# Optimization experiments

Hardware: AMD Instinct MI355X
Metric: run time of the kernel (lower is better)

Reference implementation:

```python
import jax, jax.numpy as jnp
import numpy as np

TEMP = 0.07
BASE_TEMP = 0.07
LOSS_WEIGHT = 0.5
BN_EPS = 1e-5


def _embed(x, w1, b1, gamma, beta, w2, b2):
    # 1x1 conv C->C  (x: [N,C,H,W], w1: [C_out,C_in])
    h = jnp.einsum('nchw,oc->nohw', x, w1) + b1[None, :, None, None]
    # BatchNorm2d in training mode: batch stats over (N,H,W), biased variance
    mean = h.mean(axis=(0, 2, 3), keepdims=True)
    var = h.var(axis=(0, 2, 3), keepdims=True)
    h = (h - mean) * jax.lax.rsqrt(var + BN_EPS)
    h = h * gamma[None, :, None, None] + beta[None, :, None, None]
    h = jax.nn.relu(h)
    h = jnp.einsum('nchw,oc->nohw', h, w2) + b2[None, :, None, None]
    # F.normalize(p=2, dim=1) with eps=1e-12
    nrm = jnp.sqrt(jnp.sum(h * h, axis=1, keepdims=True))
    return h / jnp.maximum(nrm, 1e-12)


def _contrastive(feats_, labels_):
    # feats_: [T, n_view, C]; labels_: [T]
    T, n_view, C = feats_.shape
    mask_small = (labels_[:, None] == labels_[None, :]).astype(feats_.dtype)  # [T,T]
    # torch.cat(torch.unbind(feats_, dim=1), dim=0): view-major ordering
    cf = feats_.transpose(1, 0, 2).reshape(T * n_view, C)
    logits = (cf @ cf.T) / TEMP                                   # [M,M], M=T*n_view
    logits = logits - jax.lax.stop_gradient(jnp.max(logits, axis=1, keepdims=True))
    mask = jnp.tile(mask_small, (n_view, n_view))                  # repeat(anchor_count, contrast_count)
    neg_mask = 1.0 - mask                                          # computed BEFORE diagonal removal
    M = T * n_view
    logits_mask = 1.0 - jnp.eye(M, dtype=feats_.dtype)
    mask = mask * logits_mask
    exp_logits = jnp.exp(logits)
    neg_logits = jnp.sum(exp_logits * neg_mask, axis=1, keepdims=True)
    log_prob = logits - jnp.log(exp_logits + neg_logits)
    mean_log_prob_pos = jnp.sum(mask * log_prob, axis=1) / (jnp.sum(mask, axis=1) + 1e-6)
    loss = -(TEMP / BASE_TEMP) * mean_log_prob_pos
    return jnp.mean(loss)


def setup_inputs() -> dict:
    N, C_in, H, W = 8, 512, 128, 128
    feat_dim, num_classes = 256, 19
    max_views, max_samples, ignore_label = 100, 1024, -1
    rng = np.random.RandomState(0)

    preds_S = rng.randn(N, C_in, H, W).astype(np.float32)
    # gt label map already at (H,W) => nearest interpolation is identity
    gt = rng.randint(0, num_classes, (N, H * W))
    logits_S = rng.randn(N, num_classes, H * W).astype(np.float32)
    predict = logits_S.argmax(axis=1)  # [N, H*W]

    # ---- replicate _hard_anchor_sampling on host (fixed seed) ----
    classes, total = [], 0
    for i in range(N):
        cl = [int(c) for c in np.unique(gt[i])
              if c != ignore_label and (gt[i] == c).sum() > max_views]
        classes.append(cl)
        total += len(cl)
    n_view = min(max_samples // total, max_views)

    b_idx, p_idx, y_cls = [], [], []
    for i in range(N):
        for c in classes[i]:
            hard = np.where((predict[i] == c) & (gt[i] != c))[0]
            easy = np.where((predict[i] == c) & (gt[i] == c))[0]
            nh, ne = len(hard), len(easy)
            if nh >= n_view / 2 and ne >= n_view / 2:
                kh = n_view // 2; ke = n_view - kh
            elif nh >= n_view / 2:
                ke = ne; kh = n_view - ke
            else:
                kh = nh; ke = n_view - kh
            hs = hard[rng.permutation(nh)[:kh]]
            es = easy[rng.permutation(ne)[:ke]]
            b_idx.append(i)
            p_idx.append(np.concatenate([hs, es]))
            y_cls.append(c)

    batch_idx = jnp.asarray(np.array(b_idx), dtype=jnp.int32)          # [T]
    pix_idx = jnp.asarray(np.stack(p_idx), dtype=jnp.int32)            # [T, n_view]
    y_cls = jnp.asarray(np.array(y_cls), dtype=jnp.int32)              # [T]

    def p(shape, scale, k):
        r = np.random.RandomState(k)
        return jnp.asarray((r.randn(*shape) * scale).astype(np.float32))

    return {
        'preds_S': jnp.asarray(preds_S),
        'w1': p((C_in, C_in), 0.02, 1),
        'b1': jnp.zeros((C_in,), jnp.float32),
        'gamma': jnp.ones((C_in,), jnp.float32),
        'beta': jnp.zeros((C_in,), jnp.float32),
        'w2': p((feat_dim, C_in), 0.02, 2),
        'b2': jnp.zeros((feat_dim,), jnp.float32),
        'batch_idx': batch_idx,
        'pix_idx': pix_idx,
        'y_cls': y_cls,
    }


def reference(preds_S, w1, b1, gamma, beta, w2, b2, batch_idx, pix_idx, y_cls):
    f = _embed(preds_S, w1, b1, gamma, beta, w2, b2)        # [N, C, H, W]
    N, C, H, W = f.shape
    feats = f.transpose(0, 2, 3, 1).reshape(N, H * W, C)     # [N, HW, C]
    X_ = feats[batch_idx[:, None], pix_idx]                   # [T, n_view, C]
    labels_ = y_cls.astype(f.dtype)
    return LOSS_WEIGHT * _contrastive(X_, labels_)
```

## Files before the change

### kernel.cpp

```cpp
#include <hip/hip_runtime.h>
#include <hip/hip_bf16.h>

#define C_IN   512
#define C_OUT  256
#define HW     16384
#define NIMG   8
#define PTOT   (NIMG * HW)
#define MP     1024
#define TEMP_INV (1.0f / 0.07f)
#define BN_EPS   1e-5f
#define SPB    4
#define OGRP   4
#define IGRP   4
#define BK     64
#define KCH    2048
#define NCHUNK (PTOT / KCH)

typedef float  f32x4  __attribute__((ext_vector_type(4)));
typedef short  short8 __attribute__((ext_vector_type(8)));
typedef short  short4v __attribute__((ext_vector_type(4)));

#define WS_S1   0
#define WS_G    (WS_S1 + NIMG * C_IN)
#define WS_W1P  (WS_G + C_IN * C_IN)
#define WS_B1P  (WS_W1P + C_IN * C_IN)
#define WS_CF   (WS_B1P + C_IN)
#define WS_XB_F (WS_CF + MP * C_OUT)
#define WS_NEED_FAST ((size_t)WS_XB_F * 4 + (size_t)PTOT * C_IN * 2)
#define WS_PART_F (WS_XB_F + PTOT * (C_IN / 2))
#define NPART_F   (10 * NCHUNK * 128 * 128)
#define WS_NEED_PART ((size_t)(WS_PART_F + NPART_F) * 4)

__global__ __launch_bounds__(256)
void kprep(const float* __restrict__ x, __hip_bfloat16* __restrict__ xb,
           float* __restrict__ s1p, float* __restrict__ out) {
    int plane = blockIdx.x;
    if (plane == 0 && threadIdx.x == 0) *out = 0.f;
    const float4* p = (const float4*)(x + (size_t)plane * HW);
    short4v* q = (short4v*)(xb + (size_t)plane * HW);
    float acc = 0.f;
    for (int i = threadIdx.x; i < HW / 4; i += 256) {
        float4 v = p[i];
        acc += v.x + v.y + v.z + v.w;
        union { short4v s; __hip_bfloat162 h[2]; } u;
        u.h[0] = __float22bfloat162_rn(make_float2(v.x, v.y));
        u.h[1] = __float22bfloat162_rn(make_float2(v.z, v.w));
        q[i] = u.s;
    }
    for (int off = 32; off; off >>= 1) acc += __shfl_down(acc, off, 64);
    __shared__ float red[4];
    int lane = threadIdx.x & 63, wv = threadIdx.x >> 6;
    if (lane == 0) red[wv] = acc;
    __syncthreads();
    if (threadIdx.x == 0)
        s1p[plane] = red[0] + red[1] + red[2] + red[3];
}

__global__ __launch_bounds__(256)
void ksum(const float* __restrict__ x, float* __restrict__ s1p, float* __restrict__ out) {
    int plane = blockIdx.x;
    if (plane == 0 && threadIdx.x == 0) *out = 0.f;
    const float4* p = (const float4*)(x + (size_t)plane * HW);
    float acc = 0.f;
    for (int i = threadIdx.x; i < HW / 4; i += 256) {
        float4 v = p[i];
        acc += v.x + v.y + v.z + v.w;
    }
    for (int off = 32; off; off >>= 1) acc += __shfl_down(acc, off, 64);
    __shared__ float red[4];
    int lane = threadIdx.x & 63, wv = threadIdx.x >> 6;
    if (lane == 0) red[wv] = acc;
    __syncthreads();
    if (threadIdx.x == 0)
        s1p[plane] = red[0] + red[1] + red[2] + red[3];
}

__device__ const int TI2[10] = {0,1,2,3, 0,0,0,1,1,2};
__device__ const int TJ2[10] = {0,1,2,3, 1,2,3,2,3,3};

template<bool PART>
__global__ __launch_bounds__(256, 3)
void kgram2(const __hip_bfloat16* __restrict__ xb, float* __restrict__ G,
            float* __restrict__ Gp) {
    __shared__ __hip_bfloat16 buf[2][128 * BK];
    int tile  = blockIdx.x;
    int IT = TI2[tile] * 128;
    int JT = TJ2[tile] * 128;
    bool diag = (IT == JT);
    int bsel = diag ? 0 : 1;
    int chunk = blockIdx.y;
    int n   = chunk >> 3;
    int hw0 = (chunk & 7) * KCH;
    int wave = threadIdx.x >> 6;
    int lane = threadIdx.x & 63;
    int wi = wave >> 1, wj = wave & 1;

    const __hip_bfloat16* gA = xb + ((size_t)n * C_IN + IT) * HW + hw0;
    const __hip_bfloat16* gB = xb + ((size_t)n * C_IN + JT) * HW + hw0;

    int rrel = lane >> 3;
    int slot = lane & 7;

    f32x4 acc[4][4];
#pragma unroll
    for (int i = 0; i < 4; ++i)
#pragma unroll
        for (int j = 0; j < 4; ++j) acc[i][j] = {0.f, 0.f, 0.f, 0.f};

    int m  = lane & 15;
    int kq = lane >> 4;

#pragma unroll 1
    for (int s = 0; s < KCH / BK; ++s) {
        int kk = s * BK;
#pragma unroll
        for (int i_ = 0; i_ < 4; ++i_) {
            int row = wave * 32 + i_ * 8 + rrel;
            int g   = slot ^ (row & 7);
            __builtin_amdgcn_global_load_lds(
                (const __attribute__((address_space(1))) void*)
                    (gA + (size_t)row * HW + kk + g * 8),
                (__attribute__((address_space(3))) void*)
                    (&buf[0][(wave * 32 + i_ * 8) * BK]),
                16, 0, 0);
            if (!diag)
                __builtin_amdgcn_global_load_lds(
                    (const __attribute__((address_space(1))) void*)
                        (gB + (size_t)row * HW + kk + g * 8),
                    (__attribute__((address_space(3))) void*)
                        (&buf[1][(wave * 32 + i_ * 8) * BK]),
                    16, 0, 0);
        }
        __syncthreads();
#pragma unroll
        for (int h = 0; h < 2; ++h) {
            short8 af[4], bf[4];
#pragma unroll
            for (int t_ = 0; t_ < 4; ++t_) {
                int ra = wi * 64 + t_ * 16 + m;
                int qa = (h * 4 + kq) ^ (ra & 7);
                af[t_] = *(const short8*)&buf[0][ra * BK + qa * 8];
                int rb = wj * 64 + t_ * 16 + m;
                int qb = (h * 4 + kq) ^ (rb & 7);
                bf[t_] = *(const short8*)&buf[bsel][rb * BK + qb * 8];
            }
#pragma unroll
            for (int i_ = 0; i_ < 4; ++i_)
#pragma unroll
                for (int j_ = 0; j_ < 4; ++j_)
                    acc[i_][j_] = __builtin_amdgcn_mfma_f32_16x16x32_bf16(
                        af[i_], bf[j_], acc[i_][j_], 0, 0, 0);
        }
        __syncthreads();
    }

    int r0 = (lane >> 4) * 4;
    int cc = lane & 15;
    if (PART) {
        float* P = Gp + ((size_t)tile * NCHUNK + chunk) * (128 * 128);
#pragma unroll
        for (int i = 0; i < 4; ++i)
#pragma unroll
            for (int j = 0; j < 4; ++j)
#pragma unroll
                for (int r = 0; r < 4; ++r)
                    P[(wi * 64 + i * 16 + r0 + r) * 128 + (wj * 64 + j * 16 + cc)]
                        = acc[i][j][r];
    } else {
#pragma unroll
        for (int i = 0; i < 4; ++i)
#pragma unroll
            for (int j = 0; j < 4; ++j)
#pragma unroll
                for (int r = 0; r < 4; ++r)
                    atomicAdd(&G[(size_t)(IT + wi * 64 + i * 16 + r0 + r) * C_IN
                                 + (JT + wj * 64 + j * 16 + cc)],
                              acc[i][j][r]);
    }
}

__global__ __launch_bounds__(256)
void kgacc(const float* __restrict__ Gp, float* __restrict__ G) {
    int tile = blockIdx.x >> 4;
    int seg  = blockIdx.x & 15;
    int IT = TI2[tile] * 128, JT = TJ2[tile] * 128;
    int e0 = seg * 1024 + threadIdx.x * 4;
    const float* base = Gp + (size_t)tile * NCHUNK * (128 * 128) + e0;
    f32x4 a0 = {0,0,0,0}, a1 = {0,0,0,0}, a2 = {0,0,0,0}, a3 = {0,0,0,0};
    for (int ch = 0; ch < NCHUNK; ch += 4) {
        a0 += *(const f32x4*)(base + (size_t)(ch + 0) * (128 * 128));
        a1 += *(const f32x4*)(base + (size_t)(ch + 1) * (128 * 128));
        a2 += *(const f32x4*)(base + (size_t)(ch + 2) * (128 * 128));
        a3 += *(const f32x4*)(base + (size_t)(ch + 3) * (128 * 128));
    }
    f32x4 s = (a0 + a1) + (a2 + a3);
    int r = e0 >> 7, c = e0 & 127;
    *(f32x4*)(&G[(size_t)(IT + r) * C_IN + JT + c]) = s;
    if (IT != JT) {
#pragma unroll
        for (int k = 0; k < 4; ++k)
            G[(size_t)(JT + c + k) * C_IN + IT + r] = s[k];
    }
}

__global__ __launch_bounds__(256)
void kmirror(float* __restrict__ G) {
    int i = blockIdx.x;
    for (int j = threadIdx.x; j < C_IN; j += 256) {
        if ((i >> 7) > (j >> 7))
            G[(size_t)i * C_IN + j] = G[(size_t)j * C_IN + i];
    }
}

__device__ inline short8 load_frag_f32(const float* p) {
    float4 a = *(const float4*)p;
    float4 b = *(const float4*)(p + 4);
    union { short8 s; __hip_bfloat162 h[4]; } u;
    u.h[0] = __float22bfloat162_rn(make_float2(a.x, a.y));
    u.h[1] = __float22bfloat162_rn(make_float2(a.z, a.w));
    u.h[2] = __float22bfloat162_rn(make_float2(b.x, b.y));
    u.h[3] = __float22bfloat162_rn(make_float2(b.z, b.w));
    return u.s;
}

__global__ __launch_bounds__(256)
void kgram_f32(const float* __restrict__ x, float* __restrict__ G) {
    int bz  = blockIdx.z;
    int n   = bz >> 2;
    int hw0 = (bz & 3) * 4096;
    int wave = threadIdx.x >> 6;
    int lane = threadIdx.x & 63;
    int wi = wave >> 1, wj = wave & 1;
    int I0 = blockIdx.x * 128 + wi * 64;
    int J0 = blockIdx.y * 128 + wj * 64;
    int m    = lane & 15;
    int koff = (lane >> 4) * 8;

    const float* baseA[4];
    const float* baseB[4];
#pragma unroll
    for (int t = 0; t < 4; ++t) {
        baseA[t] = x + ((size_t)n * C_IN + (I0 + t * 16 + m)) * HW + hw0 + koff;
        baseB[t] = x + ((size_t)n * C_IN + (J0 + t * 16 + m)) * HW + hw0 + koff;
    }

    f32x4 acc[4][4];
#pragma unroll
    for (int i = 0; i < 4; ++i)
#pragma unroll
        for (int j = 0; j < 4; ++j) acc[i][j] = {0.f, 0.f, 0.f, 0.f};

    for (int kk = 0; kk < 4096; kk += 32) {
        short8 afr[4], bfr[4];
#pragma unroll
        for (int t = 0; t < 4; ++t) {
            afr[t] = load_frag_f32(baseA[t] + kk);
            bfr[t] = load_frag_f32(baseB[t] + kk);
        }
#pragma unroll
        for (int i = 0; i < 4; ++i)
#pragma unroll
            for (int j = 0; j < 4; ++j)
                acc[i][j] = __builtin_amdgcn_mfma_f32_16x16x32_bf16(
                    afr[i], bfr[j], acc[i][j], 0, 0, 0);
    }

    int r0 = (lane >> 4) * 4;
    int cc = lane & 15;
#pragma unroll
    for (int i = 0; i < 4; ++i)
#pragma unroll
        for (int j = 0; j < 4; ++j)
#pragma unroll
            for (int r = 0; r < 4; ++r)
                atomicAdd(&G[(size_t)(I0 + i * 16 + r0 + r) * C_IN + (J0 + j * 16 + cc)],
                          acc[i][j][r]);
}

__global__ __launch_bounds__(256)
void kstats(const float* __restrict__ w1, const float* __restrict__ b1,
            const float* __restrict__ gamma, const float* __restrict__ beta,
            const float* __restrict__ s1p, const float* __restrict__ G,
            float* __restrict__ w1p, float* __restrict__ b1p) {
    int o0 = blockIdx.x * OGRP;
    int tid = threadIdx.x;
    __shared__ float wr[OGRP][C_IN];
    __shared__ float redd[4][OGRP];
    __shared__ float redq[4][OGRP];
    __shared__ float alpha_s[OGRP];

    for (int idx = tid; idx < OGRP * C_IN; idx += 256) {
        int og = idx >> 9, c = idx & (C_IN - 1);
        wr[og][c] = w1[(size_t)(o0 + og) * C_IN + c];
    }
    __syncthreads();

    float dot1[OGRP], quad[OGRP];
#pragma unroll
    for (int og = 0; og < OGRP; ++og) { dot1[og] = 0.f; quad[og] = 0.f; }

    for (int c = tid; c < C_IN; c += 256) {
        const float* gr = G + (size_t)c * C_IN;
        float s1c = 0.f;
#pragma unroll
        for (int nn = 0; nn < NIMG; ++nn) s1c += s1p[nn * C_IN + c];
        float inner[OGRP];
#pragma unroll
        for (int og = 0; og < OGRP; ++og) inner[og] = 0.f;
        for (int d = 0; d < C_IN; d += 4) {
            float4 gv = *(const float4*)(gr + d);
#pragma unroll
            for (int og = 0; og < OGRP; ++og) {
                float4 wv = *(const float4*)(&wr[og][d]);
                inner[og] += gv.x * wv.x + gv.y * wv.y + gv.z * wv.z + gv.w * wv.w;
            }
        }
#pragma unroll
        for (int og = 0; og < OGRP; ++og) {
            float wc = wr[og][c];
            quad[og] += inner[og] * wc;
            dot1[og] += s1c * wc;
        }
    }
#pragma unroll
    for (int og = 0; og < OGRP; ++og) {
        for (int off = 32; off; off >>= 1) {
            dot1[og] += __shfl_down(dot1[og], off, 64);
            quad[og] += __shfl_down(quad[og], off, 64);
        }
    }
    int lane = tid & 63, wv = tid >> 6;
    if (lane == 0) {
#pragma unroll
        for (int og = 0; og < OGRP; ++og) { redd[wv][og] = dot1[og]; redq[wv][og] = quad[og]; }
    }
    __syncthreads();
    if (tid < OGRP) {
        int og = tid;
        float d1 = redd[0][og] + redd[1][og] + redd[2][og] + redd[3][og];
        float q  = redq[0][og] + redq[1][og] + redq[2][og] + redq[3][og];
        float b  = b1[o0 + og];
        float mean = d1 / (float)PTOT + b;
        float eh2  = (q + 2.f * b * d1) / (float)PTOT + b * b;
        float var  = eh2 - mean * mean;
        float al   = gamma[o0 + og] * rsqrtf(var + BN_EPS);
        alpha_s[og] = al;
        b1p[o0 + og] = beta[o0 + og] + al * (b - mean);
    }
    __syncthreads();
    for (int idx = tid; idx < OGRP * C_IN; idx += 256) {
        int og = idx >> 9, c = idx & (C_IN - 1);
        w1p[(size_t)(o0 + og) * C_IN + c] = alpha_s[og] * wr[og][c];
    }
}

__global__ __launch_bounds__(256)
void kfeat(const float* __restrict__ x, const float* __restrict__ w1p,
           const float* __restrict__ b1p, const float* __restrict__ w2,
           const float* __restrict__ b2, const int* __restrict__ batch_idx,
           const int* __restrict__ pix_idx, float* __restrict__ cf,
           int M, int T, int n_view) {
    __shared__ float xcol[SPB][C_IN];
    __shared__ float h1[SPB][C_IN];
    __shared__ float fl[SPB][C_OUT];
    int tid = threadIdx.x;
    int m0 = blockIdx.x * SPB;

    for (int idx = tid; idx < SPB * C_IN; idx += 256) {
        int s = idx >> 9, c = idx & (C_IN - 1);
        int mm = m0 + s;
        float v = 0.f;
        if (mm < M) {
            int t = mm % T, vv = mm / T;
            int n = batch_idx[t];
            int pix = pix_idx[t * n_view + vv];
            v = x[((size_t)n * C_IN + c) * HW + pix];
        }
        xcol[s][c] = v;
    }
    __syncthreads();

    for (int o = tid; o < C_IN; o += 256) {
        float acc[SPB];
        float bb = b1p[o];
#pragma unroll
        for (int s = 0; s < SPB; ++s) acc[s] = bb;
        const float* wrp = w1p + (size_t)o * C_IN;
        for (int c = 0; c < C_IN; c += 4) {
            float4 w = *(const float4*)(wrp + c);
#pragma unroll
            for (int s = 0; s < SPB; ++s) {
                float4 xv = *(const float4*)(&xcol[s][c]);
                acc[s] += w.x * xv.x + w.y * xv.y + w.z * xv.z + w.w * xv.w;
            }
        }
#pragma unroll
        for (int s = 0; s < SPB; ++s) h1[s][o] = fmaxf(acc[s], 0.f);
    }
    __syncthreads();

    {
        int j = tid;
        float acc[SPB];
        float bb = b2[j];
#pragma unroll
        for (int s = 0; s < SPB; ++s) acc[s] = bb;
        const float* wrp = w2 + (size_t)j * C_IN;
        for (int o = 0; o < C_IN; o += 4) {
            float4 w = *(const float4*)(wrp + o);
#pragma unroll
            for (int s = 0; s < SPB; ++s) {
                float4 hv = *(const float4*)(&h1[s][o]);
                acc[s] += w.x * hv.x + w.y * hv.y + w.z * hv.z + w.w * hv.w;
            }
        }
#pragma unroll
        for (int s = 0; s < SPB; ++s) fl[s][j] = acc[s];
    }
    __syncthreads();

    int wv = tid >> 6, lane = tid & 63;
    {
        float sq = 0.f;
#pragma unroll
        for (int k = 0; k < 4; ++k) { float v = fl[wv][lane + 64 * k]; sq += v * v; }
        for (int off = 32; off; off >>= 1) sq += __shfl_down(sq, off, 64);
        float nrm = __shfl(sq, 0, 64);
        float rinv = 1.f / fmaxf(sqrtf(nrm), 1e-12f);
        int mm = m0 + wv;
        if (mm < M) {
#pragma unroll
            for (int k = 0; k < 4; ++k)
                cf[(size_t)mm * C_OUT + lane + 64 * k] = fl[wv][lane + 64 * k] * rinv;
        }
    }
}

__global__ __launch_bounds__(256)
void kloss(const float* __restrict__ cf, const int* __restrict__ y_cls,
           float* __restrict__ out, int M, int T) {
    int i0 = blockIdx.x * IGRP;
    int tid = threadIdx.x;
    __shared__ float ci[IGRP][C_OUT];
    __shared__ float row[IGRP][MP];
    __shared__ int   lbl[MP];
    __shared__ float redl[IGRP];
    int lane = tid & 63, wv = tid >> 6;

    for (int idx = tid; idx < IGRP * C_OUT; idx += 256) {
        int g = idx >> 8, c = idx & (C_OUT - 1);
        int ii = i0 + g;
        ci[g][c] = (ii < M) ? cf[(size_t)ii * C_OUT + c] : 0.f;
    }
    for (int j = tid; j < M; j += 256) lbl[j] = y_cls[j % T];
    __syncthreads();

    for (int j = tid; j < M; j += 256) {
        const float* cj = cf + (size_t)j * C_OUT;
        float acc[IGRP];
#pragma unroll
        for (int g = 0; g < IGRP; ++g) acc[g] = 0.f;
        for (int c = 0; c < C_OUT; c += 4) {
            float4 v = *(const float4*)(cj + c);
#pragma unroll
            for (int g = 0; g < IGRP; ++g) {
                float4 cv = *(const float4*)(&ci[g][c]);
                acc[g] += cv.x * v.x + cv.y * v.y + cv.z * v.z + cv.w * v.w;
            }
        }
#pragma unroll
        for (int g = 0; g < IGRP; ++g) row[g][j] = acc[g] * TEMP_INV;
    }
    __syncthreads();

    for (int g = wv; g < IGRP; g += 4) {
        int i = i0 + g;
        if (i < M) {
            int lbl_i = lbl[i];
            const float* r = row[g];

            float mx = -1e30f;
            for (int j = lane; j < M; j += 64) mx = fmaxf(mx, r[j]);
            for (int off = 32; off; off >>= 1) mx = fmaxf(mx, __shfl_down(mx, off, 64));
            mx = __shfl(mx, 0, 64);

            float neg = 0.f;
            for (int j = lane; j < M; j += 64)
                if (lbl[j] != lbl_i) neg += expf(r[j] - mx);
            for (int off = 32; off; off >>= 1) neg += __shfl_down(neg, off, 64);
            neg = __shfl(neg, 0, 64);

            float pos = 0.f; int cnt = 0;
            for (int j = lane; j < M; j += 64) {
                if (lbl[j] == lbl_i && j != i) {
                    float l = r[j] - mx;
                    pos += l - logf(expf(l) + neg);
                    cnt++;
                }
            }
            for (int off = 32; off; off >>= 1) {
                pos += __shfl_down(pos, off, 64);
                cnt += __shfl_down(cnt, off, 64);
            }
            if (lane == 0) redl[g] = -pos / ((float)cnt + 1e-6f);
        } else if (lane == 0) redl[g] = 0.f;
    }
    __syncthreads();
    if (tid == 0) {
        float s = 0.f;
        for (int g = 0; g < IGRP; ++g) s += redl[g];
        atomicAdd(out, s * (0.5f / (float)M));
    }
}

extern "C" void kernel_launch(void* const* d_in, const int* in_sizes, int n_in,
                              void* d_out, int out_size, void* d_ws, size_t ws_size,
                              hipStream_t stream) {
    const float* x     = (const float*)d_in[0];
    const float* w1    = (const float*)d_in[1];
    const float* b1    = (const float*)d_in[2];
    const float* gamma = (const float*)d_in[3];
    const float* beta  = (const float*)d_in[4];
    const float* w2    = (const float*)d_in[5];
    const float* b2    = (const float*)d_in[6];
    const int* batch_idx = (const int*)d_in[7];
    const int* pix_idx   = (const int*)d_in[8];
    const int* y_cls     = (const int*)d_in[9];

    int T = in_sizes[7];
    int M = in_sizes[8];
    int n_view = M / T;

    float* ws  = (float*)d_ws;
    float* s1p = ws + WS_S1;
    float* G   = ws + WS_G;
    float* w1p = ws + WS_W1P;
    float* b1p = ws + WS_B1P;
    float* cf  = ws + WS_CF;
    __hip_bfloat16* xb = (__hip_bfloat16*)(ws + WS_XB_F);
    float* Gpart = ws + WS_PART_F;

    if (ws_size >= WS_NEED_PART) {
        kprep<<<NIMG * C_IN, 256, 0, stream>>>(x, xb, s1p, (float*)d_out);
        kgram2<true><<<dim3(10, NCHUNK), 256, 0, stream>>>(xb, G, Gpart);
        kgacc<<<160, 256, 0, stream>>>(Gpart, G);
    } else if (ws_size >= WS_NEED_FAST) {
        hipMemsetAsync(G, 0, (size_t)(C_IN * C_IN) * sizeof(float), stream);
        kprep<<<NIMG * C_IN, 256, 0, stream>>>(x, xb, s1p, (float*)d_out);
        kgram2<false><<<dim3(10, NCHUNK), 256, 0, stream>>>(xb, G, nullptr);
        kmirror<<<C_IN, 256, 0, stream>>>(G);
    } else {
        hipMemsetAsync(G, 0, (size_t)(C_IN * C_IN) * sizeof(float), stream);
        ksum<<<NIMG * C_IN, 256, 0, stream>>>(x, s1p, (float*)d_out);
        kgram_f32<<<dim3(4, 4, 32), 256, 0, stream>>>(x, G);
    }
    kstats<<<C_IN / OGRP, 256, 0, stream>>>(w1, b1, gamma, beta, s1p, G, w1p, b1p);
    kfeat<<<(M + SPB - 1) / SPB, 256, 0, stream>>>(x, w1p, b1p, w2, b2,
                                                   batch_idx, pix_idx, cf, M, T, n_view);
    kloss<<<(M + IGRP - 1) / IGRP, 256, 0, stream>>>(cf, y_cls, (float*)d_out, M, T);
}
```

Before: 629.3 us.

## Double-buffer Gram kernel, XCD-aware block mapping, and parallelize BN stats

The partial-Gram kernel now double-buffers its LDS tiles, prefetching the next K-step while MFMAs run on the current one, and always loads separate A/B buffers. Blocks are remapped so the 8 chunks of a tile are spread across XCDs. The serial per-output kstats kernel is replaced by a 2D-parallel kquad reduction with atomics, a tiny kfin kernel, and folding of the BN scale into kfeat instead of writing a scaled W1 copy. Costs are more LDS per block (occupancy drops to 2), redundant B loads on diagonal tiles, and order-dependent float atomics.

```diff
diff --git a/kernel.cpp b/kernel.cpp
--- a/kernel.cpp
+++ b/kernel.cpp
@@ -10,32 +10,39 @@
 #define TEMP_INV (1.0f / 0.07f)
 #define BN_EPS   1e-5f
 #define SPB    4
-#define OGRP   4
 #define IGRP   4
 #define BK     64
 #define KCH    2048
 #define NCHUNK (PTOT / KCH)
+#define NTILE  10
 
 typedef float  f32x4  __attribute__((ext_vector_type(4)));
 typedef short  short8 __attribute__((ext_vector_type(8)));
 typedef short  short4v __attribute__((ext_vector_type(4)));
 
-#define WS_S1   0
-#define WS_G    (WS_S1 + NIMG * C_IN)
-#define WS_W1P  (WS_G + C_IN * C_IN)
-#define WS_B1P  (WS_W1P + C_IN * C_IN)
-#define WS_CF   (WS_B1P + C_IN)
-#define WS_XB_F (WS_CF + MP * C_OUT)
+#define WS_S1    0
+#define WS_G     (WS_S1 + NIMG * C_IN)
+#define WS_QUAD  (WS_G + C_IN * C_IN)
+#define WS_DOT1  (WS_QUAD + C_IN)
+#define WS_ALPHA (WS_DOT1 + C_IN)
+#define WS_B1P   (WS_ALPHA + C_IN)
+#define WS_CF    (WS_B1P + C_IN)
+#define WS_XB_F  (WS_CF + MP * C_OUT)
 #define WS_NEED_FAST ((size_t)WS_XB_F * 4 + (size_t)PTOT * C_IN * 2)
 #define WS_PART_F (WS_XB_F + PTOT * (C_IN / 2))
-#define NPART_F   (10 * NCHUNK * 128 * 128)
+#define NPART_F   (NTILE * NCHUNK * 128 * 128)
 #define WS_NEED_PART ((size_t)(WS_PART_F + NPART_F) * 4)
 
 __global__ __launch_bounds__(256)
 void kprep(const float* __restrict__ x, __hip_bfloat16* __restrict__ xb,
-           float* __restrict__ s1p, float* __restrict__ out) {
+           float* __restrict__ s1p, float* __restrict__ quadb,
+           float* __restrict__ dot1b, float* __restrict__ out) {
     int plane = blockIdx.x;
-    if (plane == 0 && threadIdx.x == 0) *out = 0.f;
+    if (plane == 0) {
+        if (threadIdx.x == 0) *out = 0.f;
+        quadb[threadIdx.x] = 0.f; quadb[256 + threadIdx.x] = 0.f;
+        dot1b[threadIdx.x] = 0.f; dot1b[256 + threadIdx.x] = 0.f;
+    }
     const float4* p = (const float4*)(x + (size_t)plane * HW);
     short4v* q = (short4v*)(xb + (size_t)plane * HW);
     float acc = 0.f;
@@ -57,9 +64,15 @@
 }
 
 __global__ __launch_bounds__(256)
-void ksum(const float* __restrict__ x, float* __restrict__ s1p, float* __restrict__ out) {
+void ksum(const float* __restrict__ x, float* __restrict__ s1p,
+          float* __restrict__ quadb, float* __restrict__ dot1b,
+          float* __restrict__ out) {
     int plane = blockIdx.x;
-    if (plane == 0 && threadIdx.x == 0) *out = 0.f;
+    if (plane == 0) {
+        if (threadIdx.x == 0) *out = 0.f;
+        quadb[threadIdx.x] = 0.f; quadb[256 + threadIdx.x] = 0.f;
+        dot1b[threadIdx.x] = 0.f; dot1b[256 + threadIdx.x] = 0.f;
+    }
     const float4* p = (const float4*)(x + (size_t)plane * HW);
     float acc = 0.f;
     for (int i = threadIdx.x; i < HW / 4; i += 256) {
@@ -75,31 +88,27 @@
         s1p[plane] = red[0] + red[1] + red[2] + red[3];
 }
 
-__device__ const int TI2[10] = {0,1,2,3, 0,0,0,1,1,2};
-__device__ const int TJ2[10] = {0,1,2,3, 1,2,3,2,3,3};
-
-template<bool PART>
-__global__ __launch_bounds__(256, 3)
-void kgram2(const __hip_bfloat16* __restrict__ xb, float* __restrict__ G,
-            float* __restrict__ Gp) {
-    __shared__ __hip_bfloat16 buf[2][128 * BK];
-    int tile  = blockIdx.x;
-    int IT = TI2[tile] * 128;
-    int JT = TJ2[tile] * 128;
-    bool diag = (IT == JT);
-    int bsel = diag ? 0 : 1;
-    int chunk = blockIdx.y;
+__device__ const int TI2[NTILE] = {0,1,2,3, 0,0,0,1,1,2};
+__device__ const int TJ2[NTILE] = {0,1,2,3, 1,2,3,2,3,3};
+
+__global__ __launch_bounds__(256, 2)
+void kgram3(const __hip_bfloat16* __restrict__ xb, float* __restrict__ Gp) {
+    __shared__ __hip_bfloat16 Ab[2][128 * BK];
+    __shared__ __hip_bfloat16 Bb[2][128 * BK];
+    int bid  = blockIdx.x;
+    int xcd  = bid & 7;
+    int r    = bid >> 3;
+    int tile = r % NTILE;
+    int chunk = (r / NTILE) * 8 + xcd;
+    int IT = TI2[tile] * 128, JT = TJ2[tile] * 128;
     int n   = chunk >> 3;
     int hw0 = (chunk & 7) * KCH;
-    int wave = threadIdx.x >> 6;
-    int lane = threadIdx.x & 63;
+    int wave = threadIdx.x >> 6, lane = threadIdx.x & 63;
     int wi = wave >> 1, wj = wave & 1;
-
     const __hip_bfloat16* gA = xb + ((size_t)n * C_IN + IT) * HW + hw0;
     const __hip_bfloat16* gB = xb + ((size_t)n * C_IN + JT) * HW + hw0;
-
-    int rrel = lane >> 3;
-    int slot = lane & 7;
+    int rrel = lane >> 3, slot = lane & 7;
+    int m = lane & 15, kq = lane >> 4;
 
     f32x4 acc[4][4];
 #pragma unroll
@@ -107,31 +116,24 @@
 #pragma unroll
         for (int j = 0; j < 4; ++j) acc[i][j] = {0.f, 0.f, 0.f, 0.f};
 
-    int m  = lane & 15;
-    int kq = lane >> 4;
-
-#pragma unroll 1
-    for (int s = 0; s < KCH / BK; ++s) {
-        int kk = s * BK;
+    auto stage = [&](int sel, int kk_) {
 #pragma unroll
         for (int i_ = 0; i_ < 4; ++i_) {
             int row = wave * 32 + i_ * 8 + rrel;
             int g   = slot ^ (row & 7);
             __builtin_amdgcn_global_load_lds(
                 (const __attribute__((address_space(1))) void*)
-                    (gA + (size_t)row * HW + kk + g * 8),
+                    (gA + (size_t)row * HW + kk_ + g * 8),
                 (__attribute__((address_space(3))) void*)
-                    (&buf[0][(wave * 32 + i_ * 8) * BK]),
-                16, 0, 0);
-            if (!diag)
-                __builtin_amdgcn_global_load_lds(
-                    (const __attribute__((address_space(1))) void*)
-                        (gB + (size_t)row * HW + kk + g * 8),
-                    (__attribute__((address_space(3))) void*)
-                        (&buf[1][(wave * 32 + i_ * 8) * BK]),
-                    16, 0, 0);
-        }
-        __syncthreads();
+                    (&Ab[sel][(wave * 32 + i_ * 8) * BK]), 16, 0, 0);
+            __builtin_amdgcn_global_load_lds(
+                (const __attribute__((address_space(1))) void*)
+                    (gB + (size_t)row * HW + kk_ + g * 8),
+                (__attribute__((address_space(3))) void*)
+                    (&Bb[sel][(wave * 32 + i_ * 8) * BK]), 16, 0, 0);
+        }
+    };
+    auto compute = [&](int cur) {
 #pragma unroll
         for (int h = 0; h < 2; ++h) {
             short8 af[4], bf[4];
@@ -139,10 +141,10 @@
             for (int t_ = 0; t_ < 4; ++t_) {
                 int ra = wi * 64 + t_ * 16 + m;
                 int qa = (h * 4 + kq) ^ (ra & 7);
-                af[t_] = *(const short8*)&buf[0][ra * BK + qa * 8];
+                af[t_] = *(const short8*)&Ab[cur][ra * BK + qa * 8];
                 int rb = wj * 64 + t_ * 16 + m;
                 int qb = (h * 4 + kq) ^ (rb & 7);
-                bf[t_] = *(const short8*)&buf[bsel][rb * BK + qb * 8];
+                bf[t_] = *(const short8*)&Bb[cur][rb * BK + qb * 8];
             }
 #pragma unroll
             for (int i_ = 0; i_ < 4; ++i_)
@@ -151,32 +153,36 @@
                     acc[i_][j_] = __builtin_amdgcn_mfma_f32_16x16x32_bf16(
                         af[i_], bf[j_], acc[i_][j_], 0, 0, 0);
         }
-        __syncthreads();
-    }
+    };
+
+    constexpr int NS = KCH / BK;
+    stage(0, 0);
+#pragma unroll 1
+    for (int s = 0; s < NS - 1; ++s) {
+        int cur = s & 1;
+        stage(cur ^ 1, (s + 1) * BK);
+        asm volatile("s_waitcnt vmcnt(8)" ::: "memory");
+        __builtin_amdgcn_sched_barrier(0);
+        __builtin_amdgcn_s_barrier();
+        compute(cur);
+        __builtin_amdgcn_s_barrier();
+    }
+    asm volatile("s_waitcnt vmcnt(0)" ::: "memory");
+    __builtin_amdgcn_sched_barrier(0);
+    __builtin_amdgcn_s_barrier();
+    compute((NS - 1) & 1);
 
     int r0 = (lane >> 4) * 4;
     int cc = lane & 15;
-    if (PART) {
-        float* P = Gp + ((size_t)tile * NCHUNK + chunk) * (128 * 128);
-#pragma unroll
-        for (int i = 0; i < 4; ++i)
-#pragma unroll
-            for (int j = 0; j < 4; ++j)
-#pragma unroll
-                for (int r = 0; r < 4; ++r)
-                    P[(wi * 64 + i * 16 + r0 + r) * 128 + (wj * 64 + j * 16 + cc)]
-                        = acc[i][j][r];
-    } else {
-#pragma unroll
-        for (int i = 0; i < 4; ++i)
-#pragma unroll
-            for (int j = 0; j < 4; ++j)
-#pragma unroll
-                for (int r = 0; r < 4; ++r)
-                    atomicAdd(&G[(size_t)(IT + wi * 64 + i * 16 + r0 + r) * C_IN
-                                 + (JT + wj * 64 + j * 16 + cc)],
-                              acc[i][j][r]);
-    }
+    float* P = Gp + ((size_t)tile * NCHUNK + chunk) * (128 * 128);
+#pragma unroll
+    for (int i = 0; i < 4; ++i)
+#pragma unroll
+        for (int j = 0; j < 4; ++j)
+#pragma unroll
+            for (int rr = 0; rr < 4; ++rr)
+                P[(wi * 64 + i * 16 + r0 + rr) * 128 + (wj * 64 + j * 16 + cc)]
+                    = acc[i][j][rr];
 }
 
 __global__ __launch_bounds__(256)
@@ -194,13 +200,91 @@
         a3 += *(const f32x4*)(base + (size_t)(ch + 3) * (128 * 128));
     }
     f32x4 s = (a0 + a1) + (a2 + a3);
-    int r = e0 >> 7, c = e0 & 127;
-    *(f32x4*)(&G[(size_t)(IT + r) * C_IN + JT + c]) = s;
+    int rr = e0 >> 7, c = e0 & 127;
+    *(f32x4*)(&G[(size_t)(IT + rr) * C_IN + JT + c]) = s;
     if (IT != JT) {
 #pragma unroll
         for (int k = 0; k < 4; ++k)
-            G[(size_t)(JT + c + k) * C_IN + IT + r] = s[k];
-    }
+            G[(size_t)(JT + c + k) * C_IN + IT + rr] = s[k];
+    }
+}
+
+__global__ __launch_bounds__(256, 3)
+void kgram_at(const __hip_bfloat16* __restrict__ xb, float* __restrict__ G) {
+    __shared__ __hip_bfloat16 buf[2][128 * BK];
+    int tile  = blockIdx.x;
+    int IT = TI2[tile] * 128, JT = TJ2[tile] * 128;
+    bool diag = (IT == JT);
+    int bsel = diag ? 0 : 1;
+    int chunk = blockIdx.y;
+    int n   = chunk >> 3;
+    int hw0 = (chunk & 7) * KCH;
+    int wave = threadIdx.x >> 6, lane = threadIdx.x & 63;
+    int wi = wave >> 1, wj = wave & 1;
+    const __hip_bfloat16* gA = xb + ((size_t)n * C_IN + IT) * HW + hw0;
+    const __hip_bfloat16* gB = xb + ((size_t)n * C_IN + JT) * HW + hw0;
+    int rrel = lane >> 3, slot = lane & 7;
+    int m = lane & 15, kq = lane >> 4;
+
+    f32x4 acc[4][4];
+#pragma unroll
+    for (int i = 0; i < 4; ++i)
+#pragma unroll
+        for (int j = 0; j < 4; ++j) acc[i][j] = {0.f, 0.f, 0.f, 0.f};
+
+#pragma unroll 1
+    for (int s = 0; s < KCH / BK; ++s) {
+        int kk = s * BK;
+#pragma unroll
+        for (int i_ = 0; i_ < 4; ++i_) {
+            int row = wave * 32 + i_ * 8 + rrel;
+            int g   = slot ^ (row & 7);
+            __builtin_amdgcn_global_load_lds(
+                (const __attribute__((address_space(1))) void*)
+                    (gA + (size_t)row * HW + kk + g * 8),
+                (__attribute__((address_space(3))) void*)
+                    (&buf[0][(wave * 32 + i_ * 8) * BK]), 16, 0, 0);
+            if (!diag)
+                __builtin_amdgcn_global_load_lds(
+                    (const __attribute__((address_space(1))) void*)
+                        (gB + (size_t)row * HW + kk + g * 8),
+                    (__attribute__((address_space(3))) void*)
+                        (&buf[1][(wave * 32 + i_ * 8) * BK]), 16, 0, 0);
+        }
+        __syncthreads();
+#pragma unroll
+        for (int h = 0; h < 2; ++h) {
+            short8 af[4], bf[4];
+#pragma unroll
+            for (int t_ = 0; t_ < 4; ++t_) {
+                int ra = wi * 64 + t_ * 16 + m;
+                int qa = (h * 4 + kq) ^ (ra & 7);
+                af[t_] = *(const short8*)&buf[0][ra * BK + qa * 8];
+                int rb = wj * 64 + t_ * 16 + m;
+                int qb = (h * 4 + kq) ^ (rb & 7);
+                bf[t_] = *(const short8*)&buf[bsel][rb * BK + qb * 8];
+            }
+#pragma unroll
+            for (int i_ = 0; i_ < 4; ++i_)
+#pragma unroll
+                for (int j_ = 0; j_ < 4; ++j_)
+                    acc[i_][j_] = __builtin_amdgcn_mfma_f32_16x16x32_bf16(
+                        af[i_], bf[j_], acc[i_][j_], 0, 0, 0);
+        }
+        __syncthreads();
+    }
+
+    int r0 = (lane >> 4) * 4;
+    int cc = lane & 15;
+#pragma unroll
+    for (int i = 0; i < 4; ++i)
+#pragma unroll
+        for (int j = 0; j < 4; ++j)
+#pragma unroll
+            for (int rr = 0; rr < 4; ++rr)
+                atomicAdd(&G[(size_t)(IT + wi * 64 + i * 16 + r0 + rr) * C_IN
+                             + (JT + wj * 64 + j * 16 + cc)],
+                          acc[i][j][rr]);
 }
 
 __global__ __launch_bounds__(256)
@@ -228,8 +312,7 @@
     int bz  = blockIdx.z;
     int n   = bz >> 2;
     int hw0 = (bz & 3) * 4096;
-    int wave = threadIdx.x >> 6;
-    int lane = threadIdx.x & 63;
+    int wave = threadIdx.x >> 6, lane = threadIdx.x & 63;
     int wi = wave >> 1, wj = wave & 1;
     int I0 = blockIdx.x * 128 + wi * 64;
     int J0 = blockIdx.y * 128 + wj * 64;
@@ -272,94 +355,86 @@
 #pragma unroll
         for (int j = 0; j < 4; ++j)
 #pragma unroll
-            for (int r = 0; r < 4; ++r)
-                atomicAdd(&G[(size_t)(I0 + i * 16 + r0 + r) * C_IN + (J0 + j * 16 + cc)],
-                          acc[i][j][r]);
-}
-
-__global__ __launch_bounds__(256)
-void kstats(const float* __restrict__ w1, const float* __restrict__ b1,
-            const float* __restrict__ gamma, const float* __restrict__ beta,
-            const float* __restrict__ s1p, const float* __restrict__ G,
-            float* __restrict__ w1p, float* __restrict__ b1p) {
-    int o0 = blockIdx.x * OGRP;
+            for (int rr = 0; rr < 4; ++rr)
+                atomicAdd(&G[(size_t)(I0 + i * 16 + r0 + rr) * C_IN + (J0 + j * 16 + cc)],
+                          acc[i][j][rr]);
+}
+
+__global__ __launch_bounds__(256)
+void kquad(const float* __restrict__ G, const float* __restrict__ w1,
+           const float* __restrict__ s1p, float* __restrict__ quadb,
+           float* __restrict__ dot1b) {
+    __shared__ float Wt[16][516];
+    __shared__ float pq[16], pd1[16], s1t[32];
     int tid = threadIdx.x;
-    __shared__ float wr[OGRP][C_IN];
-    __shared__ float redd[4][OGRP];
-    __shared__ float redq[4][OGRP];
-    __shared__ float alpha_s[OGRP];
-
-    for (int idx = tid; idx < OGRP * C_IN; idx += 256) {
-        int og = idx >> 9, c = idx & (C_IN - 1);
-        wr[og][c] = w1[(size_t)(o0 + og) * C_IN + c];
-    }
-    __syncthreads();
-
-    float dot1[OGRP], quad[OGRP];
-#pragma unroll
-    for (int og = 0; og < OGRP; ++og) { dot1[og] = 0.f; quad[og] = 0.f; }
-
-    for (int c = tid; c < C_IN; c += 256) {
-        const float* gr = G + (size_t)c * C_IN;
-        float s1c = 0.f;
-#pragma unroll
-        for (int nn = 0; nn < NIMG; ++nn) s1c += s1p[nn * C_IN + c];
-        float inner[OGRP];
-#pragma unroll
-        for (int og = 0; og < OGRP; ++og) inner[og] = 0.f;
-        for (int d = 0; d < C_IN; d += 4) {
-            float4 gv = *(const float4*)(gr + d);
-#pragma unroll
-            for (int og = 0; og < OGRP; ++og) {
-                float4 wv = *(const float4*)(&wr[og][d]);
-                inner[og] += gv.x * wv.x + gv.y * wv.y + gv.z * wv.z + gv.w * wv.w;
-            }
-        }
-#pragma unroll
-        for (int og = 0; og < OGRP; ++og) {
-            float wc = wr[og][c];
-            quad[og] += inner[og] * wc;
-            dot1[og] += s1c * wc;
-        }
-    }
-#pragma unroll
-    for (int og = 0; og < OGRP; ++og) {
-        for (int off = 32; off; off >>= 1) {
-            dot1[og] += __shfl_down(dot1[og], off, 64);
-            quad[og] += __shfl_down(quad[og], off, 64);
-        }
-    }
-    int lane = tid & 63, wv = tid >> 6;
-    if (lane == 0) {
-#pragma unroll
-        for (int og = 0; og < OGRP; ++og) { redd[wv][og] = dot1[og]; redq[wv][og] = quad[og]; }
-    }
-    __syncthreads();
-    if (tid < OGRP) {
-        int og = tid;
-        float d1 = redd[0][og] + redd[1][og] + redd[2][og] + redd[3][og];
-        float q  = redq[0][og] + redq[1][og] + redq[2][og] + redq[3][og];
-        float b  = b1[o0 + og];
-        float mean = d1 / (float)PTOT + b;
-        float eh2  = (q + 2.f * b * d1) / (float)PTOT + b * b;
-        float var  = eh2 - mean * mean;
-        float al   = gamma[o0 + og] * rsqrtf(var + BN_EPS);
-        alpha_s[og] = al;
-        b1p[o0 + og] = beta[o0 + og] + al * (b - mean);
-    }
-    __syncthreads();
-    for (int idx = tid; idx < OGRP * C_IN; idx += 256) {
-        int og = idx >> 9, c = idx & (C_IN - 1);
-        w1p[(size_t)(o0 + og) * C_IN + c] = alpha_s[og] * wr[og][c];
-    }
-}
-
-__global__ __launch_bounds__(256)
-void kfeat(const float* __restrict__ x, const float* __restrict__ w1p,
-           const float* __restrict__ b1p, const float* __restrict__ w2,
-           const float* __restrict__ b2, const int* __restrict__ batch_idx,
-           const int* __restrict__ pix_idx, float* __restrict__ cf,
-           int M, int T, int n_view) {
+    int c0 = blockIdx.x * 32, o0 = blockIdx.y * 16;
+
+    for (int idx = tid; idx < 16 * 128; idx += 256) {
+        int row = idx >> 7, c4 = idx & 127;
+        *(f32x4*)&Wt[row][c4 * 4] =
+            *(const f32x4*)(w1 + (size_t)(o0 + row) * C_IN + c4 * 4);
+    }
+    if (tid < 16) { pq[tid] = 0.f; pd1[tid] = 0.f; }
+    if (tid < 32) {
+        float s = 0.f;
+#pragma unroll
+        for (int nn = 0; nn < NIMG; ++nn) s += s1p[nn * C_IN + c0 + tid];
+        s1t[tid] = s;
+    }
+    __syncthreads();
+
+    int c_l = tid >> 3;
+    int og  = tid & 7;
+    const float* Gr = G + (size_t)(c0 + c_l) * C_IN;
+
+    f32x4 y4[2];
+#pragma unroll
+    for (int k = 0; k < 2; ++k) y4[k] = {0.f, 0.f, 0.f, 0.f};
+#pragma unroll 4
+    for (int d = 0; d < C_IN; d += 4) {
+        f32x4 g4 = *(const f32x4*)(Gr + d);
+#pragma unroll
+        for (int k = 0; k < 2; ++k)
+            y4[k] += g4 * (*(const f32x4*)&Wt[og + 8 * k][d]);
+    }
+
+    int c = c0 + c_l;
+#pragma unroll
+    for (int k = 0; k < 2; ++k) {
+        int ol = og + 8 * k;
+        float y  = y4[k][0] + y4[k][1] + y4[k][2] + y4[k][3];
+        float wc = Wt[ol][c];
+        atomicAdd(&pq[ol],  y * wc);
+        atomicAdd(&pd1[ol], s1t[c_l] * wc);
+    }
+    __syncthreads();
+    if (tid < 16) {
+        atomicAdd(&quadb[o0 + tid], pq[tid]);
+        atomicAdd(&dot1b[o0 + tid], pd1[tid]);
+    }
+}
+
+__global__ __launch_bounds__(512)
+void kfin(const float* __restrict__ quadb, const float* __restrict__ dot1b,
+          const float* __restrict__ b1, const float* __restrict__ gamma,
+          const float* __restrict__ beta, float* __restrict__ alpha,
+          float* __restrict__ b1p) {
+    int o = threadIdx.x;
+    float d1 = dot1b[o], q = quadb[o], b = b1[o];
+    float mean = d1 / (float)PTOT + b;
+    float eh2  = (q + 2.f * b * d1) / (float)PTOT + b * b;
+    float var  = eh2 - mean * mean;
+    float al   = gamma[o] * rsqrtf(var + BN_EPS);
+    alpha[o] = al;
+    b1p[o] = beta[o] + al * (b - mean);
+}
+
+__global__ __launch_bounds__(256)
+void kfeat(const float* __restrict__ x, const float* __restrict__ w1,
+           const float* __restrict__ alpha, const float* __restrict__ b1p,
+           const float* __restrict__ w2, const float* __restrict__ b2,
+           const int* __restrict__ batch_idx, const int* __restrict__ pix_idx,
+           float* __restrict__ cf, int M, int T, int n_view) {
     __shared__ float xcol[SPB][C_IN];
     __shared__ float h1[SPB][C_IN];
     __shared__ float fl[SPB][C_OUT];
@@ -382,10 +457,9 @@
 
     for (int o = tid; o < C_IN; o += 256) {
         float acc[SPB];
-        float bb = b1p[o];
-#pragma unroll
-        for (int s = 0; s < SPB; ++s) acc[s] = bb;
-        const float* wrp = w1p + (size_t)o * C_IN;
+#pragma unroll
+        for (int s = 0; s < SPB; ++s) acc[s] = 0.f;
+        const float* wrp = w1 + (size_t)o * C_IN;
         for (int c = 0; c < C_IN; c += 4) {
             float4 w = *(const float4*)(wrp + c);
 #pragma unroll
@@ -394,8 +468,9 @@
                 acc[s] += w.x * xv.x + w.y * xv.y + w.z * xv.z + w.w * xv.w;
             }
         }
-#pragma unroll
-        for (int s = 0; s < SPB; ++s) h1[s][o] = fmaxf(acc[s], 0.f);
+        float al = alpha[o], bb = b1p[o];
+#pragma unroll
+        for (int s = 0; s < SPB; ++s) h1[s][o] = fmaxf(al * acc[s] + bb, 0.f);
     }
     __syncthreads();
 
@@ -531,31 +606,34 @@
     int M = in_sizes[8];
     int n_view = M / T;
 
-    float* ws  = (float*)d_ws;
-    float* s1p = ws + WS_S1;
-    float* G   = ws + WS_G;
-    float* w1p = ws + WS_W1P;
-    float* b1p = ws + WS_B1P;
-    float* cf  = ws + WS_CF;
+    float* ws    = (float*)d_ws;
+    float* s1p   = ws + WS_S1;
+    float* G     = ws + WS_G;
+    float* quadb = ws + WS_QUAD;
+    float* dot1b = ws + WS_DOT1;
+    float* alpha = ws + WS_ALPHA;
+    float* b1p   = ws + WS_B1P;
+    float* cf    = ws + WS_CF;
     __hip_bfloat16* xb = (__hip_bfloat16*)(ws + WS_XB_F);
     float* Gpart = ws + WS_PART_F;
 
     if (ws_size >= WS_NEED_PART) {
-        kprep<<<NIMG * C_IN, 256, 0, stream>>>(x, xb, s1p, (float*)d_out);
-        kgram2<true><<<dim3(10, NCHUNK), 256, 0, stream>>>(xb, G, Gpart);
+        kprep<<<NIMG * C_IN, 256, 0, stream>>>(x, xb, s1p, quadb, dot1b, (float*)d_out);
+        kgram3<<<NTILE * NCHUNK, 256, 0, stream>>>(xb, Gpart);
         kgacc<<<160, 256, 0, stream>>>(Gpart, G);
     } else if (ws_size >= WS_NEED_FAST) {
         hipMemsetAsync(G, 0, (size_t)(C_IN * C_IN) * sizeof(float), stream);
-        kprep<<<NIMG * C_IN, 256, 0, stream>>>(x, xb, s1p, (float*)d_out);
-        kgram2<false><<<dim3(10, NCHUNK), 256, 0, stream>>>(xb, G, nullptr);
+        kprep<<<NIMG * C_IN, 256, 0, stream>>>(x, xb, s1p, quadb, dot1b, (float*)d_out);
+        kgram_at<<<dim3(NTILE, NCHUNK), 256, 0, stream>>>(xb, G);
         kmirror<<<C_IN, 256, 0, stream>>>(G);
     } else {
         hipMemsetAsync(G, 0, (size_t)(C_IN * C_IN) * sizeof(float), stream);
-        ksum<<<NIMG * C_IN, 256, 0, stream>>>(x, s1p, (float*)d_out);
+        ksum<<<NIMG * C_IN, 256, 0, stream>>>(x, s1p, quadb, dot1b, (float*)d_out);
         kgram_f32<<<dim3(4, 4, 32), 256, 0, stream>>>(x, G);
     }
-    kstats<<<C_IN / OGRP, 256, 0, stream>>>(w1, b1, gamma, beta, s1p, G, w1p, b1p);
-    kfeat<<<(M + SPB - 1) / SPB, 256, 0, stream>>>(x, w1p, b1p, w2, b2,
+    kquad<<<dim3(16, 32), 256, 0, stream>>>(G, w1, s1p, quadb, dot1b);
+    kfin<<<1, 512, 0, stream>>>(quadb, dot1b, b1, gamma, beta, alpha, b1p);
+    kfeat<<<(M + SPB - 1) / SPB, 256, 0, stream>>>(x, w1, alpha, b1p, w2, b2,
                                                    batch_idx, pix_idx, cf, M, T, n_view);
     kloss<<<(M + IGRP - 1) / IGRP, 256, 0, stream>>>(cf, y_cls, (float*)d_out, M, T);
 }
```

After: 622.4 us. About the same (-1.1%).
